# Kernel tuning notes

Measured on AMD Instinct MI355X. Metric: run time of the kernel, lower is better.

Reference implementation:

```python
import jax, jax.numpy as jnp
import numpy as np
from jax.scipy.linalg import expm

ORDER = 256
SEQ_LEN = 4096
THETA = 4096.0
MEMORY_D = 4
INPUT_SIZE = 256
HIDDEN = 512
BATCH = 8


def _lmu_AB(order):
    # Continuous-time LMU (Legendre) state-space matrices
    q = np.arange(order, dtype=np.float64)
    r = 2.0 * q + 1.0
    i, j = np.meshgrid(q, q, indexing="ij")
    A = np.where(i < j, -1.0, (-1.0) ** (i - j + 1)) * r[:, None]
    B = ((-1.0) ** q * r)[:, None]
    return A, B


def _discretize_zoh(A, B, dt=1.0):
    # ZOH via augmented matrix exponential: expm([[A,B],[0,0]]*dt)
    n = A.shape[0]
    M = np.zeros((n + 1, n + 1))
    M[:n, :n] = A * dt
    M[:n, n:] = B * dt
    Md = expm(jnp.asarray(M, dtype=jnp.float64) if jax.config.jax_enable_x64 else jnp.asarray(M, dtype=jnp.float32))
    return Md[:n, :n].astype(jnp.float32), Md[:n, n:].astype(jnp.float32)


def _impulse_H(order, seq_len, theta):
    A, B = _lmu_AB(order)
    Ad, Bd = _discretize_zoh(A / theta, B / theta, 1.0)

    def step(A_i, _):
        # H_t = A^t B ; emit A_i @ Bd then advance A_i <- Ad @ A_i
        return Ad @ A_i, (A_i @ Bd)[:, 0]

    _, Hs = jax.lax.scan(step, jnp.eye(order, dtype=jnp.float32), None, length=seq_len)
    return Hs.T  # [order, seq_len]


def setup_inputs() -> dict:
    key = jax.random.key(0)
    k1, k2, k3, k4, k5 = jax.random.split(key, 5)
    x = jax.random.normal(k1, (BATCH, SEQ_LEN, INPUT_SIZE), dtype=jnp.float32)
    Wu_w = jax.random.normal(k2, (MEMORY_D, INPUT_SIZE), dtype=jnp.float32) * (1.0 / np.sqrt(INPUT_SIZE))
    Wu_b = jax.random.normal(k3, (MEMORY_D,), dtype=jnp.float32) * 0.01
    msz = MEMORY_D * ORDER + INPUT_SIZE
    Wh_w = jax.random.normal(k4, (HIDDEN, msz), dtype=jnp.float32) * (1.0 / np.sqrt(msz))
    Wh_b = jax.random.normal(k5, (HIDDEN,), dtype=jnp.float32) * 0.01
    H = _impulse_H(ORDER, SEQ_LEN, THETA)  # exact LMU impulse response buffer
    return {"x": x, "Wu_w": Wu_w, "Wu_b": Wu_b, "Wh_w": Wh_w, "Wh_b": Wh_b, "H": H}


def reference(x, Wu_w, Wu_b, Wh_w, Wh_b, H):
    B, L, _ = x.shape
    u = jax.nn.relu(x @ Wu_w.T + Wu_b)                     # [B, L, memory_d]
    fft_u = jnp.fft.rfft(u.transpose(0, 2, 1), n=2 * L, axis=-1)   # [B, md, L+1]
    fft_H = jnp.fft.rfft(H, n=2 * L, axis=-1)              # [order, L+1]
    temp = fft_u[:, :, None, :] * fft_H[None, None, :, :]  # [B, md, order, L+1]
    m = jnp.fft.irfft(temp, n=2 * L, axis=-1)[..., :L]     # [B, md, order, L]
    m = m.reshape(B, -1, L).transpose(0, 2, 1)             # [B, L, md*order]
    input_h = jnp.concatenate([m, x], axis=-1)             # [B, L, md*order + input]
    h = jax.nn.relu(input_h @ Wh_w.T + Wh_b)               # [B, L, hidden]
    return h, h[:, -1, :]
```

## Files before the change

### kernel.cpp

```cpp
#include <hip/hip_runtime.h>

#define NB 8
#define LSEQ 4096
#define INS 256
#define MD 4
#define ORD 256
#define HID 512
#define MSZ 1280
#define FS 4128
#define NSPEC 8256
#define GMT 1056768
#define GNT 16384

#define PD(n) ((n) + ((n) >> 5))
#define LDSN 4224

typedef __attribute__((ext_vector_type(8))) short short8;
typedef __attribute__((ext_vector_type(4))) float floatx4;
typedef __attribute__((ext_vector_type(2))) float v2f;

struct ush4 { unsigned short x, y, z, w; };

__device__ v2f g_tw4096[4096];
__device__ v2f g_tw8192[4098];

__device__ __forceinline__ unsigned short f2bf(float f) {
    unsigned u = __float_as_uint(f);
    u += 0x7FFF + ((u >> 16) & 1);
    return (unsigned short)(u >> 16);
}
__device__ __forceinline__ ush4 pack4(float4 v) {
    ush4 p; p.x = f2bf(v.x); p.y = f2bf(v.y); p.z = f2bf(v.z); p.w = f2bf(v.w); return p;
}
__device__ __forceinline__ float bf2f(unsigned short s) {
    return __uint_as_float(((unsigned)s) << 16);
}

__device__ __forceinline__ v2f make2(float x, float y) { v2f r; r.x = x; r.y = y; return r; }

__device__ __forceinline__ v2f cadd(v2f a, v2f b) { return a + b; }
__device__ __forceinline__ v2f csub(v2f a, v2f b) { return a - b; }

template <int DIR>
__device__ __forceinline__ v2f jmul(v2f z) {
    const v2f s = __builtin_shufflevector(z, z, 1, 0);
    return (DIR < 0) ? s * make2(1.f, -1.f) : s * make2(-1.f, 1.f);
}

__device__ __forceinline__ v2f cmul(v2f a, v2f b) {
    const v2f byx = __builtin_shufflevector(b, b, 1, 0);
    const v2f axx = make2(a.x, a.x);
    const v2f any = make2(-a.y, a.y);
    return axx * b + any * byx;
}

template <int DIR>
__device__ __forceinline__ void bfly8(const v2f* a, v2f* b) {
    const v2f e0 = a[0] + a[4], e1 = a[0] - a[4];
    const v2f e2 = a[2] + a[6], e3 = jmul<DIR>(a[2] - a[6]);
    const v2f E0 = e0 + e2, E2 = e0 - e2;
    const v2f E1 = e1 + e3, E3 = e1 - e3;
    const v2f f0 = a[1] + a[5], f1 = a[1] - a[5];
    const v2f f2 = a[3] + a[7], f3 = jmul<DIR>(a[3] - a[7]);
    const v2f O0 = f0 + f2, O2 = f0 - f2;
    const v2f O1 = f1 + f3, O3 = f1 - f3;
    constexpr float C707 = 0.70710678118654752440f;
    const v2f W1 = make2(C707, DIR * C707);
    const v2f W3 = make2(-C707, DIR * C707);
    const v2f T1 = cmul(O1, W1);
    const v2f T2 = jmul<DIR>(O2);
    const v2f T3 = cmul(O3, W3);
    b[0] = E0 + O0; b[4] = E0 - O0;
    b[1] = E1 + T1; b[5] = E1 - T1;
    b[2] = E2 + T2; b[6] = E2 - T2;
    b[3] = E3 + T3; b[7] = E3 - T3;
}

template <int DIR, int N_, int S_>
__device__ __forceinline__ void fft_stage_ip(v2f* __restrict__ X, int tid) {
    constexpr int M_ = N_ / 8;
    constexpr int STEP = 4096 / N_;
    const int q = tid & (S_ - 1);
    const int p = tid / S_;
    const int rb = q + S_ * p;
    v2f a[8], b[8];
#pragma unroll
    for (int l = 0; l < 8; ++l) a[l] = X[PD(rb + S_ * l * M_)];

    const int pw = p * STEP;
    v2f w[7];
#pragma unroll
    for (int j = 1; j <= 7; ++j) {
        v2f t = g_tw4096[pw * j];
        if (DIR > 0) t.y = -t.y;
        w[j - 1] = t;
    }

    bfly8<DIR>(a, b);

    __syncthreads();

    const int wb = q + S_ * 8 * p;
    X[PD(wb + 0 * S_)] = b[0];
#pragma unroll
    for (int j = 1; j < 8; ++j)
        X[PD(wb + j * S_)] = cmul(b[j], w[j - 1]);
    __syncthreads();
}

extern "C" __global__ __launch_bounds__(256) void u_relu_k(
    const float* __restrict__ x, const float* __restrict__ Wuw,
    const float* __restrict__ Wub, float* __restrict__ u_t,
    unsigned short* __restrict__ x_bf,
    const float* __restrict__ Whw, unsigned short* __restrict__ Whw_bf,
    unsigned short* __restrict__ Wt) {
    const int blk = blockIdx.x;
    if (blk >= 8832) {
        if (blk < 8848) {
            const int i = (blk - 8832) * 256 + threadIdx.x;
            float sn, cs;
            sincosf(-1.53398078788564403e-3f * (float)i, &sn, &cs);
            g_tw4096[i] = make2(cs, sn);
        } else {
            const int i = (blk - 8848) * 256 + threadIdx.x;
            if (i <= 4097) {
                float sn, cs;
                sincosf(-7.66990393942820614e-4f * (float)i, &sn, &cs);
                g_tw8192[i] = make2(cs, sn);
            }
        }
        return;
    }
    if (blk >= 8704) {
        const int didx = (blk - 8704) * 1024 + threadIdx.x * 4;
        const int c = didx >> 14;
        const int r = didx & 16383;
        const int h = r >> 5, kk = r & 31;
        const float4 v = *(const float4*)(Whw + (size_t)h * MSZ + 1024 + c * 32 + kk);
        *(ush4*)(&Wt[didx]) = pack4(v);
        return;
    }
    if (blk >= 8192) {
        const int idx = (blk - 8192) * 256 + threadIdx.x;
        const int h = idx >> 8, c = idx & 255;
        const float4 v = ((const float4*)Whw)[(size_t)h * 320 + c];
        *(ush4*)(&Whw_bf[(size_t)idx * 4]) = pack4(v);
        return;
    }
    const int gid = blk * 256 + threadIdx.x;
    const int row = gid >> 6;
    const int lane = threadIdx.x & 63;
    const float4 xv = ((const float4*)x)[(size_t)row * 64 + lane];
    unsigned d0 = (unsigned)f2bf(xv.x) | ((unsigned)f2bf(xv.y) << 16);
    unsigned d1 = (unsigned)f2bf(xv.z) | ((unsigned)f2bf(xv.w) << 16);
    const unsigned e0 = (unsigned)__shfl_xor((int)d0, 1);
    const unsigned e1 = (unsigned)__shfl_xor((int)d1, 1);
    if (!(lane & 1)) {
        uint4 v; v.x = d0; v.y = d1; v.z = e0; v.w = e1;
        *(uint4*)(&x_bf[(size_t)row * 256 + lane * 4]) = v;
    }
    const float4 w0 = ((const float4*)Wuw)[0 * 64 + lane];
    const float4 w1 = ((const float4*)Wuw)[1 * 64 + lane];
    const float4 w2 = ((const float4*)Wuw)[2 * 64 + lane];
    const float4 w3 = ((const float4*)Wuw)[3 * 64 + lane];
    float a0 = xv.x * w0.x + xv.y * w0.y + xv.z * w0.z + xv.w * w0.w;
    float a1 = xv.x * w1.x + xv.y * w1.y + xv.z * w1.z + xv.w * w1.w;
    float a2 = xv.x * w2.x + xv.y * w2.y + xv.z * w2.z + xv.w * w2.w;
    float a3 = xv.x * w3.x + xv.y * w3.y + xv.z * w3.z + xv.w * w3.w;
#pragma unroll
    for (int off = 1; off < 64; off <<= 1) {
        a0 += __shfl_xor(a0, off);
        a1 += __shfl_xor(a1, off);
        a2 += __shfl_xor(a2, off);
        a3 += __shfl_xor(a3, off);
    }
    if (lane < 4) {
        float v = (lane == 0) ? a0 : (lane == 1) ? a1 : (lane == 2) ? a2 : a3;
        v = fmaxf(v + Wub[lane], 0.0f);
        const int b = row >> 12, t = row & 4095;
        u_t[((size_t)(b * 4 + lane)) * LSEQ + t] = v;
    }
}

extern "C" __global__ __launch_bounds__(512) void rfft_all_k(
    const float* __restrict__ ut, const float* __restrict__ H,
    v2f* __restrict__ fftU, unsigned short* __restrict__ fftHB) {
    __shared__ v2f A[LDSN];
    const int blk = blockIdx.x;
    const int tid = threadIdx.x;
    const bool is_u = (blk < 32);
    const float* src = is_u ? (ut + (size_t)blk * LSEQ) : (H + (size_t)(blk - 32) * LSEQ);
    const v2f* rp = (const v2f*)src;
    {
        v2f c[8], b[8];
#pragma unroll
        for (int j = 0; j < 4; ++j) c[j] = rp[tid + j * 512];
#pragma unroll
        for (int j = 4; j < 8; ++j) c[j] = make2(0.f, 0.f);
        bfly8<-1>(c, b);
        A[PD(8 * tid + 0)] = b[0];
#pragma unroll
        for (int j = 1; j < 8; ++j)
            A[PD(8 * tid + j)] = cmul(b[j], g_tw4096[tid * j]);
    }
    __syncthreads();
    fft_stage_ip<-1, 512, 8>(A, tid);
    fft_stage_ip<-1, 64, 64>(A, tid);
    fft_stage_ip<-1, 8, 512>(A, tid);
    if (is_u) {
        v2f* op = fftU + (size_t)blk * FS;
#pragma unroll
        for (int j = 0; j < 9; ++j) {
            const int k = tid + j * 512;
            if (k <= 4096) {
                const v2f Zk = A[PD(k & 4095)];
                const v2f Zm = A[PD((4096 - k) & 4095)];
                const v2f Zm2 = Zm * make2(1.f, -1.f);
                const v2f E = (Zk + Zm2) * 0.5f;
                const v2f D = (Zk - Zm2) * 0.5f;
                const v2f O = jmul<-1>(D);
                const v2f t = g_tw8192[k];
                op[k] = E + cmul(t, O);
            }
        }
    } else {
        const int o = blk - 32;
        unsigned* op = (unsigned*)(fftHB + (size_t)o * NSPEC);
#pragma unroll
        for (int j = 0; j < 9; ++j) {
            const int k = tid + j * 512;
            if (k <= 4096) {
                const v2f Zk = A[PD(k & 4095)];
                const v2f Zm = A[PD((4096 - k) & 4095)];
                const v2f Zm2 = Zm * make2(1.f, -1.f);
                const v2f E = (Zk + Zm2) * 0.5f;
                const v2f D = (Zk - Zm2) * 0.5f;
                const v2f O = jmul<-1>(D);
                const v2f t = g_tw8192[k];
                const v2f c = E + cmul(t, O);
                if (2 * k < NSPEC)
                    op[k] = (unsigned)f2bf(c.x) | ((unsigned)f2bf(c.y) << 16);
            }
        }
    }
}

extern "C" __global__ __launch_bounds__(256) void ht2_k(
    const unsigned short* __restrict__ fftHB, unsigned short* __restrict__ fftHT) {
    __shared__ unsigned short T[64 * 68];
    const int tid = threadIdx.x;
    const int s0 = blockIdx.x * 64;
    const int o0 = blockIdx.y * 64;
    const int r = tid >> 4, c4 = (tid & 15) * 4;
#pragma unroll
    for (int i = 0; i < 4; ++i) {
        const int o = r + 16 * i;
        const ush4 v = *(const ush4*)(fftHB + (size_t)(o0 + o) * NSPEC + s0 + c4);
        *(ush4*)(&T[o * 68 + c4]) = v;
    }
    __syncthreads();
#pragma unroll
    for (int i = 0; i < 4; ++i) {
        const int sl = r + 16 * i;
        const int s = s0 + sl;
        ush4 p;
        if (s < 8194) {
            p.x = T[(c4 + 0) * 68 + sl];
            p.y = T[(c4 + 1) * 68 + sl];
            p.z = T[(c4 + 2) * 68 + sl];
            p.w = T[(c4 + 3) * 68 + sl];
        } else { p.x = p.y = p.z = p.w = 0; }
        *(ush4*)(&fftHT[(size_t)s * 256 + o0 + c4]) = p;
    }
}

extern "C" __global__ __launch_bounds__(256) void g_gemm_k(
    const unsigned short* __restrict__ Whw_bf, const unsigned short* __restrict__ fftHT,
    unsigned short* __restrict__ fftG) {
    __shared__ __align__(16) char smem[36864];
    short* As = (short*)smem;
    short* Bs = (short*)(smem + 18432);
    short* Tt = (short*)smem;

    const int tid = threadIdx.x, lane = tid & 63, wave = tid >> 6;
    const int wg = blockIdx.x;
    const int loc = wg >> 3;
    const int mt = (wg & 7) * 2 + (loc & 1);
    const int nt = loc >> 1;
    const int m0 = mt * 128;
    const int n0 = nt * 128;
    floatx4 acc[2][8];
#pragma unroll
    for (int i = 0; i < 2; ++i)
#pragma unroll
        for (int j = 0; j < 8; ++j) acc[i][j] = (floatx4){0.f, 0.f, 0.f, 0.f};

    const int lr = tid >> 3;
    const int lc = (tid & 7) * 8;
    short8 ra[4], rb[4];

#define GL_A(kc, i) (*(const short8*)(Whw_bf + (size_t)((m0 + lr + 32 * (i)) >> 2) * 1024 + ((m0 + lr + 32 * (i)) & 3) * 256 + (kc) * 64 + lc))
#pragma unroll
    for (int i = 0; i < 4; ++i) {
        ra[i] = GL_A(0, i);
        const int n = n0 + lr + 32 * i;
        rb[i] = (n < NSPEC) ? *(const short8*)(fftHT + (size_t)n * 256 + lc)
                            : (short8){0, 0, 0, 0, 0, 0, 0, 0};
    }

    for (int kc = 0; kc < 4; ++kc) {
#pragma unroll
        for (int i = 0; i < 4; ++i) {
            *(short8*)(&As[(lr + 32 * i) * 72 + lc]) = ra[i];
            *(short8*)(&Bs[(lr + 32 * i) * 72 + lc]) = rb[i];
        }
        __syncthreads();
        if (kc < 3) {
#pragma unroll
            for (int i = 0; i < 4; ++i) {
                ra[i] = GL_A(kc + 1, i);
                const int n = n0 + lr + 32 * i;
                rb[i] = (n < NSPEC) ? *(const short8*)(fftHT + (size_t)n * 256 + (kc + 1) * 64 + lc)
                                    : (short8){0, 0, 0, 0, 0, 0, 0, 0};
            }
        }
        const int arow = (wave * 32 + (lane & 15)) * 72;
        const int brow = (lane & 15) * 72;
        const int kq = 8 * (lane >> 4);
#pragma unroll
        for (int kk = 0; kk < 2; ++kk) {
            const int ko = kk * 32 + kq;
            const short8 a0 = *(const short8*)(&As[arow + ko]);
            const short8 a1 = *(const short8*)(&As[arow + 16 * 72 + ko]);
#pragma unroll
            for (int nf = 0; nf < 8; ++nf) {
                const short8 bv = *(const short8*)(&Bs[brow + nf * 16 * 72 + ko]);
                acc[0][nf] = __builtin_amdgcn_mfma_f32_16x16x32_bf16(a0, bv, acc[0][nf], 0, 0, 0);
                acc[1][nf] = __builtin_amdgcn_mfma_f32_16x16x32_bf16(a1, bv, acc[1][nf], 0, 0, 0);
            }
        }
        __syncthreads();
    }
#undef GL_A
    const int wm = wave * 32;
#pragma unroll
    for (int mf = 0; mf < 2; ++mf) {
        const int row = wm + mf * 16 + 4 * (lane >> 4);
#pragma unroll
        for (int nf = 0; nf < 8; ++nf) {
            const int col = nf * 16 + (lane & 15);
#pragma unroll
            for (int r = 0; r < 4; ++r)
                Tt[(row + r) * 136 + col] = (short)f2bf(acc[mf][nf][r]);
        }
    }
    __syncthreads();
    const size_t gb = (size_t)mt * GMT + (size_t)nt * GNT;
    if (n0 < 8192) {
#pragma unroll
        for (int i = 0; i < 8; ++i) {
            const int idx = tid + i * 256;
            const int ml = idx >> 4, c8 = (idx & 15) * 8;
            const short8 v = *(const short8*)(&Tt[ml * 136 + c8]);
            *(short8*)(&fftG[gb + (size_t)idx * 8]) = v;
        }
    } else {
#pragma unroll
        for (int i = 0; i < 4; ++i) {
            const int idx = tid + i * 256;
            const int ml = idx >> 3, c8 = (idx & 7) * 8;
            const short8 v = *(const short8*)(&Tt[ml * 136 + c8]);
            *(short8*)(&fftG[gb + (size_t)idx * 8]) = v;
        }
    }
}

extern "C" __global__ __launch_bounds__(512) void conv_ifft_k(
    const v2f* __restrict__ fftU, const unsigned short* __restrict__ fftG,
    unsigned short* __restrict__ y) {
    __shared__ v2f A[LDSN];
    __shared__ v2f S4096;
    const int wg = blockIdx.x;
    const int h = ((wg & 7) << 6) + (wg >> 6);
    const int b = (wg >> 3) & 7;
    const int tid = threadIdx.x;
    const v2f* U = fftU + (size_t)b * MD * FS;
    const size_t mbase = (size_t)(h >> 5) * GMT + (size_t)((h & 31) * 4) * 128;
    const size_t tail = (size_t)(h >> 5) * GMT + (size_t)64 * GNT + (size_t)((h & 31) * 4) * 64;
#pragma unroll
    for (int j = 0; j < 9; ++j) {
        const int k = tid + j * 512;
        if (k <= 4096) {
            v2f s = make2(0.f, 0.f);
#pragma unroll
            for (int d = 0; d < MD; ++d) {
                const unsigned gv = (k < 4096)
                    ? *(const unsigned*)(fftG + mbase + (size_t)d * 128 + (size_t)(k >> 6) * GNT + (k & 63) * 2)
                    : *(const unsigned*)(fftG + tail + (size_t)d * 64);
                const v2f uu = U[d * FS + k];
                const float gx = __uint_as_float(gv << 16);
                const float gy = __uint_as_float(gv & 0xFFFF0000u);
                s.x = fmaf(uu.x, gx, fmaf(-uu.y, gy, s.x));
                s.y = fmaf(uu.x, gy, fmaf(uu.y, gx, s.y));
            }
            if (k < 4096) A[PD(k)] = s;
            else S4096 = s;
        }
    }
    __syncthreads();
    v2f c[8], bt[8];
#pragma unroll
    for (int j = 0; j < 8; ++j) {
        const int k = tid + j * 512;
        const v2f Sk = A[PD(k)];
        const v2f Sm = (k == 0) ? S4096 : A[PD(4096 - k)];
        const v2f Sm2 = Sm * make2(1.f, -1.f);
        const v2f E = (Sk + Sm2) * 0.5f;
        const v2f D = (Sk - Sm2) * 0.5f;
        const v2f t = g_tw8192[k];
        const v2f tc = t * make2(1.f, -1.f);
        const v2f O = cmul(D, tc);
        c[j] = E + jmul<1>(O);
    }
    __syncthreads();
    bfly8<1>(c, bt);
    A[PD(8 * tid + 0)] = bt[0];
#pragma unroll
    for (int j = 1; j < 8; ++j) {
        v2f t = g_tw4096[tid * j]; t.y = -t.y;
        A[PD(8 * tid + j)] = cmul(bt[j], t);
    }
    __syncthreads();
    fft_stage_ip<1, 512, 8>(A, tid);
    fft_stage_ip<1, 64, 64>(A, tid);
    {
        v2f z[8], bo[8];
#pragma unroll
        for (int k = 0; k < 8; ++k) z[k] = A[PD(tid + 512 * k)];
        bfly8<1>(z, bo);
        const float inv = 1.0f / 4096.0f;
#pragma unroll
        for (int k = 0; k < 4; ++k)
            A[PD(tid + 512 * k)] = bo[k] * inv;
    }
    __syncthreads();
    unsigned short* yp = y + (size_t)(b * HID + h) * LSEQ;
    {
        const int q = tid;
        unsigned dw[4];
#pragma unroll
        for (int jj = 0; jj < 4; ++jj) {
            const v2f z = A[PD(4 * q + jj)];
            dw[jj] = (unsigned)f2bf(z.x) | ((unsigned)f2bf(z.y) << 16);
        }
        uint4 v; v.x = dw[0]; v.y = dw[1]; v.z = dw[2]; v.w = dw[3];
        *(uint4*)(yp + 8 * q) = v;
    }
}

extern "C" __global__ __launch_bounds__(256) void out_gemm_k(
    const unsigned short* __restrict__ x_bf, const unsigned short* __restrict__ Wt,
    const float* __restrict__ Whb, const unsigned short* __restrict__ y,
    float* __restrict__ out) {
    __shared__ __align__(16) char smem[66560];
    short* As = (short*)smem;
    short* Bs = (short*)(smem + 2560);
    float* Whbs = (float*)smem;
    short* Ys = (short*)(smem + 2560);
    float* Ct = (float*)smem;

    const int tid = threadIdx.x, lane = tid & 63, wave = tid >> 6;
    const int wg = blockIdx.x;
    const int s = ((wg & 7) << 7) + (wg >> 3);
    const int m0 = s * 32;
    const int b = m0 >> 12;
    const int t0 = m0 & 4095;
    const int hq = wave * 128;

    floatx4 acc[2][8];
#pragma unroll
    for (int i = 0; i < 2; ++i)
#pragma unroll
        for (int j = 0; j < 8; ++j) acc[i][j] = (floatx4){0.f, 0.f, 0.f, 0.f};

    short8 ra, rb[8];
    const int arow = tid >> 2, acb = (tid & 3) * 8;
    if (tid < 128) ra = *(const short8*)(x_bf + (size_t)(m0 + arow) * INS + acb);
#pragma unroll
    for (int j = 0; j < 8; ++j)
        rb[j] = *(const short8*)(Wt + (size_t)tid * 64 + j * 8);

    for (int c = 0; c < 8; ++c) {
        if (tid < 128) *(short8*)(&As[arow * 40 + acb]) = ra;
#pragma unroll
        for (int j = 0; j < 8; ++j)
            *(short8*)(&Bs[(2 * tid + (j >> 2)) * 40 + (j & 3) * 8]) = rb[j];
        __syncthreads();
        if (c < 7) {
            if (tid < 128) ra = *(const short8*)(x_bf + (size_t)(m0 + arow) * INS + (c + 1) * 32 + acb);
#pragma unroll
            for (int j = 0; j < 8; ++j)
                rb[j] = *(const short8*)(Wt + (size_t)(c + 1) * 16384 + (size_t)tid * 64 + j * 8);
        }
        const int kq = 8 * (lane >> 4);
        const short8 a0 = *(const short8*)(&As[(lane & 15) * 40 + kq]);
        const short8 a1 = *(const short8*)(&As[((lane & 15) + 16) * 40 + kq]);
#pragma unroll
        for (int nf = 0; nf < 8; ++nf) {
            const short8 bv = *(const short8*)(&Bs[(hq + nf * 16 + (lane & 15)) * 40 + kq]);
            acc[0][nf] = __builtin_amdgcn_mfma_f32_16x16x32_bf16(a0, bv, acc[0][nf], 0, 0, 0);
            acc[1][nf] = __builtin_amdgcn_mfma_f32_16x16x32_bf16(a1, bv, acc[1][nf], 0, 0, 0);
        }
        __syncthreads();
    }

    Whbs[tid] = Whb[tid];
    Whbs[tid + 256] = Whb[tid + 256];
#pragma unroll
    for (int i = 0; i < 16; ++i) {
        const int idx = tid + i * 256;
        const int hh = idx >> 3, tq = (idx & 7) * 4;
        const ush4 v = *(const ush4*)(y + (size_t)(b * HID + hh) * LSEQ + t0 + tq);
        *(ush4*)(&Ys[hh * 36 + tq]) = v;
    }
    __syncthreads();
#pragma unroll
    for (int nf = 0; nf < 8; ++nf) {
        const int hh = hq + nf * 16 + (lane & 15);
        const float bias = Whbs[hh];
#pragma unroll
        for (int mf = 0; mf < 2; ++mf)
#pragma unroll
            for (int r = 0; r < 4; ++r) {
                const int row = mf * 16 + 4 * (lane >> 4) + r;
                acc[mf][nf][r] = fmaxf(acc[mf][nf][r] + bf2f(Ys[hh * 36 + row]) + bias, 0.f);
            }
    }
    __syncthreads();
#pragma unroll
    for (int nf = 0; nf < 8; ++nf) {
        const int col = hq + nf * 16 + (lane & 15);
#pragma unroll
        for (int mf = 0; mf < 2; ++mf)
#pragma unroll
            for (int r = 0; r < 4; ++r) {
                const int row = mf * 16 + 4 * (lane >> 4) + r;
                Ct[row * 520 + col] = acc[mf][nf][r];
            }
    }
    __syncthreads();
#pragma unroll
    for (int i = 0; i < 16; ++i) {
        const int idx = tid + i * 256;
        const int row = idx >> 7, c4 = (idx & 127) * 4;
        const floatx4 t = *(const floatx4*)&Ct[row * 520 + c4];
        *(floatx4*)(out + (size_t)(m0 + row) * HID + c4) = t;
        if (((m0 + row) & 4095) == 4095)
            *(floatx4*)(out + (size_t)NB * LSEQ * HID + (size_t)b * HID + c4) = t;
    }
}

extern "C" void kernel_launch(void* const* d_in, const int* in_sizes, int n_in,
                              void* d_out, int out_size, void* d_ws, size_t ws_size,
                              hipStream_t stream) {
    const float* x   = (const float*)d_in[0];
    const float* Wuw = (const float*)d_in[1];
    const float* Wub = (const float*)d_in[2];
    const float* Whw = (const float*)d_in[3];
    const float* Whb = (const float*)d_in[4];
    const float* H   = (const float*)d_in[5];
    char* wsb = (char*)d_ws;
    unsigned short* fftG   = (unsigned short*)(wsb);
    unsigned short* yb     = (unsigned short*)(wsb + 33816576);
    v2f*            fftU   = (v2f*)(wsb + 67371008);
    unsigned short* fftHT  = (unsigned short*)(wsb + 68427776);
    float*          ut     = (float*)(wsb + 72654848);
    unsigned short* x_bf   = (unsigned short*)(wsb + 73179136);
    unsigned short* Whw_bf = (unsigned short*)(wsb + 89956352);
    unsigned short* Wt     = (unsigned short*)(wsb + 91004928);
    unsigned short* fftHB  = (unsigned short*)(wsb + 91267072);
    float* out = (float*)d_out;

    hipLaunchKernelGGL(u_relu_k, dim3(8865), dim3(256), 0, stream, x, Wuw, Wub, ut, x_bf, Whw, Whw_bf, Wt);
    hipLaunchKernelGGL(rfft_all_k, dim3(288), dim3(512), 0, stream, ut, H, fftU, fftHB);
    hipLaunchKernelGGL(ht2_k, dim3(129, 4), dim3(256), 0, stream, fftHB, fftHT);
    hipLaunchKernelGGL(g_gemm_k, dim3(1040), dim3(256), 0, stream, Whw_bf, fftHT, fftG);
    hipLaunchKernelGGL(conv_ifft_k, dim3(4096), dim3(512), 0, stream, fftU, fftG, yb);
    hipLaunchKernelGGL(out_gemm_k, dim3(1024), dim3(256), 0, stream, x_bf, Wt, Whb, yb, out);
}
```

Baseline: 246.7 us.

## Regroup prep kernels into stages and use packed f32/bf16 conversion instructions

Regroups the front-end launches. A small prep kernel converts the weights and builds the twiddle tables. The H rfft now runs in the same launch as the x projection and bf16 conversion, and the u rfft runs with the H spectrum transpose. This overlaps independent work, keeps the launch count the same, and drops one dependency barrier between launches. It also swaps manual bf16 rounding for v_cvt_pk_bf16_f32 and uses inline-asm packed add/fma in the butterflies, which may limit compiler scheduling.

```diff
diff --git a/kernel.cpp b/kernel.cpp
--- a/kernel.cpp
+++ b/kernel.cpp
@@ -35,18 +35,27 @@
 __device__ __forceinline__ float bf2f(unsigned short s) {
     return __uint_as_float(((unsigned)s) << 16);
 }
+__device__ __forceinline__ unsigned cvt_pk_bf16(float lo, float hi) {
+    unsigned r;
+    asm("v_cvt_pk_bf16_f32 %0, %1, %2" : "=v"(r) : "v"(lo), "v"(hi));
+    return r;
+}
 
 __device__ __forceinline__ v2f make2(float x, float y) { v2f r; r.x = x; r.y = y; return r; }
 
-__device__ __forceinline__ v2f cadd(v2f a, v2f b) { return a + b; }
-__device__ __forceinline__ v2f csub(v2f a, v2f b) { return a - b; }
+__device__ __forceinline__ v2f padd(v2f a, v2f b) {
+    v2f r; asm("v_pk_add_f32 %0, %1, %2" : "=v"(r) : "v"(a), "v"(b)); return r;
+}
+__device__ __forceinline__ v2f psub(v2f a, v2f b) {
+    const v2f m1 = make2(-1.f, -1.f);
+    v2f r; asm("v_pk_fma_f32 %0, %1, %2, %3" : "=v"(r) : "v"(b), "v"(m1), "v"(a)); return r;
+}
 
 template <int DIR>
 __device__ __forceinline__ v2f jmul(v2f z) {
     const v2f s = __builtin_shufflevector(z, z, 1, 0);
     return (DIR < 0) ? s * make2(1.f, -1.f) : s * make2(-1.f, 1.f);
 }
-
 __device__ __forceinline__ v2f cmul(v2f a, v2f b) {
     const v2f byx = __builtin_shufflevector(b, b, 1, 0);
     const v2f axx = make2(a.x, a.x);
@@ -56,24 +65,24 @@
 
 template <int DIR>
 __device__ __forceinline__ void bfly8(const v2f* a, v2f* b) {
-    const v2f e0 = a[0] + a[4], e1 = a[0] - a[4];
-    const v2f e2 = a[2] + a[6], e3 = jmul<DIR>(a[2] - a[6]);
-    const v2f E0 = e0 + e2, E2 = e0 - e2;
-    const v2f E1 = e1 + e3, E3 = e1 - e3;
-    const v2f f0 = a[1] + a[5], f1 = a[1] - a[5];
-    const v2f f2 = a[3] + a[7], f3 = jmul<DIR>(a[3] - a[7]);
-    const v2f O0 = f0 + f2, O2 = f0 - f2;
-    const v2f O1 = f1 + f3, O3 = f1 - f3;
+    const v2f e0 = padd(a[0], a[4]), e1 = psub(a[0], a[4]);
+    const v2f e2 = padd(a[2], a[6]), e3 = jmul<DIR>(psub(a[2], a[6]));
+    const v2f E0 = padd(e0, e2), E2 = psub(e0, e2);
+    const v2f E1 = padd(e1, e3), E3 = psub(e1, e3);
+    const v2f f0 = padd(a[1], a[5]), f1 = psub(a[1], a[5]);
+    const v2f f2 = padd(a[3], a[7]), f3 = jmul<DIR>(psub(a[3], a[7]));
+    const v2f O0 = padd(f0, f2), O2 = psub(f0, f2);
+    const v2f O1 = padd(f1, f3), O3 = psub(f1, f3);
     constexpr float C707 = 0.70710678118654752440f;
     const v2f W1 = make2(C707, DIR * C707);
     const v2f W3 = make2(-C707, DIR * C707);
     const v2f T1 = cmul(O1, W1);
     const v2f T2 = jmul<DIR>(O2);
     const v2f T3 = cmul(O3, W3);
-    b[0] = E0 + O0; b[4] = E0 - O0;
-    b[1] = E1 + T1; b[5] = E1 - T1;
-    b[2] = E2 + T2; b[6] = E2 - T2;
-    b[3] = E3 + T3; b[7] = E3 - T3;
+    b[0] = padd(E0, O0); b[4] = psub(E0, O0);
+    b[1] = padd(E1, T1); b[5] = psub(E1, T1);
+    b[2] = padd(E2, T2); b[6] = psub(E2, T2);
+    b[3] = padd(E3, T3); b[7] = psub(E3, T3);
 }
 
 template <int DIR, int N_, int S_>
@@ -108,51 +117,88 @@
     __syncthreads();
 }
 
-extern "C" __global__ __launch_bounds__(256) void u_relu_k(
-    const float* __restrict__ x, const float* __restrict__ Wuw,
-    const float* __restrict__ Wub, float* __restrict__ u_t,
-    unsigned short* __restrict__ x_bf,
+extern "C" __global__ __launch_bounds__(256) void prep_k(
     const float* __restrict__ Whw, unsigned short* __restrict__ Whw_bf,
     unsigned short* __restrict__ Wt) {
     const int blk = blockIdx.x;
-    if (blk >= 8832) {
-        if (blk < 8848) {
-            const int i = (blk - 8832) * 256 + threadIdx.x;
-            float sn, cs;
-            sincosf(-1.53398078788564403e-3f * (float)i, &sn, &cs);
-            g_tw4096[i] = make2(cs, sn);
-        } else {
-            const int i = (blk - 8848) * 256 + threadIdx.x;
-            if (i <= 4097) {
-                float sn, cs;
-                sincosf(-7.66990393942820614e-4f * (float)i, &sn, &cs);
-                g_tw8192[i] = make2(cs, sn);
-            }
-        }
-        return;
-    }
-    if (blk >= 8704) {
-        const int didx = (blk - 8704) * 1024 + threadIdx.x * 4;
+    if (blk < 512) {
+        const int idx = blk * 256 + threadIdx.x;
+        const int h = idx >> 8, c = idx & 255;
+        const float4 v = ((const float4*)Whw)[(size_t)h * 320 + c];
+        *(ush4*)(&Whw_bf[(size_t)idx * 4]) = pack4(v);
+    } else if (blk < 640) {
+        const int didx = (blk - 512) * 1024 + threadIdx.x * 4;
         const int c = didx >> 14;
         const int r = didx & 16383;
         const int h = r >> 5, kk = r & 31;
         const float4 v = *(const float4*)(Whw + (size_t)h * MSZ + 1024 + c * 32 + kk);
         *(ush4*)(&Wt[didx]) = pack4(v);
+    } else if (blk < 656) {
+        const int i = (blk - 640) * 256 + threadIdx.x;
+        float sn, cs;
+        sincosf(-1.53398078788564403e-3f * (float)i, &sn, &cs);
+        g_tw4096[i] = make2(cs, sn);
+    } else {
+        const int i = (blk - 656) * 256 + threadIdx.x;
+        if (i <= 4097) {
+            float sn, cs;
+            sincosf(-7.66990393942820614e-4f * (float)i, &sn, &cs);
+            g_tw8192[i] = make2(cs, sn);
+        }
+    }
+}
+
+extern "C" __global__ __launch_bounds__(512) void stage1_k(
+    const float* __restrict__ x, const float* __restrict__ Wuw,
+    const float* __restrict__ Wub, float* __restrict__ u_t,
+    unsigned short* __restrict__ x_bf,
+    const float* __restrict__ H, unsigned short* __restrict__ fftHB) {
+    const int blk = blockIdx.x;
+    const int tid = threadIdx.x;
+    if (blk < 256) {
+        __shared__ v2f A[LDSN];
+        const int o = blk;
+        const v2f* rp = (const v2f*)(H + (size_t)o * LSEQ);
+        {
+            v2f c[8], b[8];
+#pragma unroll
+            for (int j = 0; j < 4; ++j) c[j] = rp[tid + j * 512];
+#pragma unroll
+            for (int j = 4; j < 8; ++j) c[j] = make2(0.f, 0.f);
+            bfly8<-1>(c, b);
+            A[PD(8 * tid + 0)] = b[0];
+#pragma unroll
+            for (int j = 1; j < 8; ++j)
+                A[PD(8 * tid + j)] = cmul(b[j], g_tw4096[tid * j]);
+        }
+        __syncthreads();
+        fft_stage_ip<-1, 512, 8>(A, tid);
+        fft_stage_ip<-1, 64, 64>(A, tid);
+        fft_stage_ip<-1, 8, 512>(A, tid);
+        unsigned* op = (unsigned*)(fftHB + (size_t)o * NSPEC);
+#pragma unroll
+        for (int j = 0; j < 9; ++j) {
+            const int k = tid + j * 512;
+            if (k <= 4096) {
+                const v2f Zk = A[PD(k & 4095)];
+                const v2f Zm = A[PD((4096 - k) & 4095)];
+                const v2f Zm2 = Zm * make2(1.f, -1.f);
+                const v2f E = padd(Zk, Zm2) * 0.5f;
+                const v2f D = psub(Zk, Zm2) * 0.5f;
+                const v2f O = jmul<-1>(D);
+                const v2f t = g_tw8192[k];
+                const v2f c = padd(E, cmul(t, O));
+                if (2 * k < NSPEC)
+                    op[k] = cvt_pk_bf16(c.x, c.y);
+            }
+        }
         return;
     }
-    if (blk >= 8192) {
-        const int idx = (blk - 8192) * 256 + threadIdx.x;
-        const int h = idx >> 8, c = idx & 255;
-        const float4 v = ((const float4*)Whw)[(size_t)h * 320 + c];
-        *(ush4*)(&Whw_bf[(size_t)idx * 4]) = pack4(v);
-        return;
-    }
-    const int gid = blk * 256 + threadIdx.x;
-    const int row = gid >> 6;
-    const int lane = threadIdx.x & 63;
+    const int row = (blk - 256) * 8 + (tid >> 6);
+    const int lane = tid & 63;
     const float4 xv = ((const float4*)x)[(size_t)row * 64 + lane];
-    unsigned d0 = (unsigned)f2bf(xv.x) | ((unsigned)f2bf(xv.y) << 16);
-    unsigned d1 = (unsigned)f2bf(xv.z) | ((unsigned)f2bf(xv.w) << 16);
+    unsigned d0 = cvt_pk_bf16(xv.x, xv.y);
+    unsigned d1 = cvt_pk_bf16(xv.z, xv.w);
     const unsigned e0 = (unsigned)__shfl_xor((int)d0, 1);
     const unsigned e1 = (unsigned)__shfl_xor((int)d1, 1);
     if (!(lane & 1)) {
@@ -182,32 +228,30 @@
     }
 }
 
-extern "C" __global__ __launch_bounds__(512) void rfft_all_k(
-    const float* __restrict__ ut, const float* __restrict__ H,
-    v2f* __restrict__ fftU, unsigned short* __restrict__ fftHB) {
-    __shared__ v2f A[LDSN];
+extern "C" __global__ __launch_bounds__(512) void stage2_k(
+    const float* __restrict__ ut, v2f* __restrict__ fftU,
+    const unsigned short* __restrict__ fftHB, unsigned short* __restrict__ fftHT) {
     const int blk = blockIdx.x;
     const int tid = threadIdx.x;
-    const bool is_u = (blk < 32);
-    const float* src = is_u ? (ut + (size_t)blk * LSEQ) : (H + (size_t)(blk - 32) * LSEQ);
-    const v2f* rp = (const v2f*)src;
-    {
-        v2f c[8], b[8];
-#pragma unroll
-        for (int j = 0; j < 4; ++j) c[j] = rp[tid + j * 512];
-#pragma unroll
-        for (int j = 4; j < 8; ++j) c[j] = make2(0.f, 0.f);
-        bfly8<-1>(c, b);
-        A[PD(8 * tid + 0)] = b[0];
-#pragma unroll
-        for (int j = 1; j < 8; ++j)
-            A[PD(8 * tid + j)] = cmul(b[j], g_tw4096[tid * j]);
-    }
-    __syncthreads();
-    fft_stage_ip<-1, 512, 8>(A, tid);
-    fft_stage_ip<-1, 64, 64>(A, tid);
-    fft_stage_ip<-1, 8, 512>(A, tid);
-    if (is_u) {
+    if (blk < 32) {
+        __shared__ v2f A[LDSN];
+        const v2f* rp = (const v2f*)(ut + (size_t)blk * LSEQ);
+        {
+            v2f c[8], b[8];
+#pragma unroll
+            for (int j = 0; j < 4; ++j) c[j] = rp[tid + j * 512];
+#pragma unroll
+            for (int j = 4; j < 8; ++j) c[j] = make2(0.f, 0.f);
+            bfly8<-1>(c, b);
+            A[PD(8 * tid + 0)] = b[0];
+#pragma unroll
+            for (int j = 1; j < 8; ++j)
+                A[PD(8 * tid + j)] = cmul(b[j], g_tw4096[tid * j]);
+        }
+        __syncthreads();
+        fft_stage_ip<-1, 512, 8>(A, tid);
+        fft_stage_ip<-1, 64, 64>(A, tid);
+        fft_stage_ip<-1, 8, 512>(A, tid);
         v2f* op = fftU + (size_t)blk * FS;
 #pragma unroll
         for (int j = 0; j < 9; ++j) {
@@ -216,47 +260,27 @@
                 const v2f Zk = A[PD(k & 4095)];
                 const v2f Zm = A[PD((4096 - k) & 4095)];
                 const v2f Zm2 = Zm * make2(1.f, -1.f);
-                const v2f E = (Zk + Zm2) * 0.5f;
-                const v2f D = (Zk - Zm2) * 0.5f;
+                const v2f E = padd(Zk, Zm2) * 0.5f;
+                const v2f D = psub(Zk, Zm2) * 0.5f;
                 const v2f O = jmul<-1>(D);
                 const v2f t = g_tw8192[k];
-                op[k] = E + cmul(t, O);
+                op[k] = padd(E, cmul(t, O));
             }
         }
-    } else {
-        const int o = blk - 32;
-        unsigned* op = (unsigned*)(fftHB + (size_t)o * NSPEC);
-#pragma unroll
-        for (int j = 0; j < 9; ++j) {
-            const int k = tid + j * 512;
-            if (k <= 4096) {
-                const v2f Zk = A[PD(k & 4095)];
-                const v2f Zm = A[PD((4096 - k) & 4095)];
-                const v2f Zm2 = Zm * make2(1.f, -1.f);
-                const v2f E = (Zk + Zm2) * 0.5f;
-                const v2f D = (Zk - Zm2) * 0.5f;
-                const v2f O = jmul<-1>(D);
-                const v2f t = g_tw8192[k];
-                const v2f c = E + cmul(t, O);
-                if (2 * k < NSPEC)
-                    op[k] = (unsigned)f2bf(c.x) | ((unsigned)f2bf(c.y) << 16);
-            }
-        }
-    }
-}
-
-extern "C" __global__ __launch_bounds__(256) void ht2_k(
-    const unsigned short* __restrict__ fftHB, unsigned short* __restrict__ fftHT) {
-    __shared__ unsigned short T[64 * 68];
-    const int tid = threadIdx.x;
-    const int s0 = blockIdx.x * 64;
-    const int o0 = blockIdx.y * 64;
-    const int r = tid >> 4, c4 = (tid & 15) * 4;
+        return;
+    }
+    __shared__ unsigned short T[2][64 * 68];
+    const int sub = tid >> 8;
+    const int tt = tid & 255;
+    const int t = (blk - 32) * 2 + sub;
+    const int s0 = (t % 129) * 64;
+    const int o0 = (t / 129) * 64;
+    const int r = tt >> 4, c4 = (tt & 15) * 4;
 #pragma unroll
     for (int i = 0; i < 4; ++i) {
         const int o = r + 16 * i;
         const ush4 v = *(const ush4*)(fftHB + (size_t)(o0 + o) * NSPEC + s0 + c4);
-        *(ush4*)(&T[o * 68 + c4]) = v;
+        *(ush4*)(&T[sub][o * 68 + c4]) = v;
     }
     __syncthreads();
 #pragma unroll
@@ -265,10 +289,10 @@
         const int s = s0 + sl;
         ush4 p;
         if (s < 8194) {
-            p.x = T[(c4 + 0) * 68 + sl];
-            p.y = T[(c4 + 1) * 68 + sl];
-            p.z = T[(c4 + 2) * 68 + sl];
-            p.w = T[(c4 + 3) * 68 + sl];
+            p.x = T[sub][(c4 + 0) * 68 + sl];
+            p.y = T[sub][(c4 + 1) * 68 + sl];
+            p.z = T[sub][(c4 + 2) * 68 + sl];
+            p.w = T[sub][(c4 + 3) * 68 + sl];
         } else { p.x = p.y = p.z = p.w = 0; }
         *(ush4*)(&fftHT[(size_t)s * 256 + o0 + c4]) = p;
     }
@@ -415,12 +439,12 @@
         const v2f Sk = A[PD(k)];
         const v2f Sm = (k == 0) ? S4096 : A[PD(4096 - k)];
         const v2f Sm2 = Sm * make2(1.f, -1.f);
-        const v2f E = (Sk + Sm2) * 0.5f;
-        const v2f D = (Sk - Sm2) * 0.5f;
+        const v2f E = padd(Sk, Sm2) * 0.5f;
+        const v2f D = psub(Sk, Sm2) * 0.5f;
         const v2f t = g_tw8192[k];
         const v2f tc = t * make2(1.f, -1.f);
         const v2f O = cmul(D, tc);
-        c[j] = E + jmul<1>(O);
+        c[j] = padd(E, jmul<1>(O));
     }
     __syncthreads();
     bfly8<1>(c, bt);
@@ -451,7 +475,7 @@
 #pragma unroll
         for (int jj = 0; jj < 4; ++jj) {
             const v2f z = A[PD(4 * q + jj)];
-            dw[jj] = (unsigned)f2bf(z.x) | ((unsigned)f2bf(z.y) << 16);
+            dw[jj] = cvt_pk_bf16(z.x, z.y);
         }
         uint4 v; v.x = dw[0]; v.y = dw[1]; v.z = dw[2]; v.w = dw[3];
         *(uint4*)(yp + 8 * q) = v;
@@ -581,9 +605,9 @@
     unsigned short* fftHB  = (unsigned short*)(wsb + 91267072);
     float* out = (float*)d_out;
 
-    hipLaunchKernelGGL(u_relu_k, dim3(8865), dim3(256), 0, stream, x, Wuw, Wub, ut, x_bf, Whw, Whw_bf, Wt);
-    hipLaunchKernelGGL(rfft_all_k, dim3(288), dim3(512), 0, stream, ut, H, fftU, fftHB);
-    hipLaunchKernelGGL(ht2_k, dim3(129, 4), dim3(256), 0, stream, fftHB, fftHT);
+    hipLaunchKernelGGL(prep_k, dim3(673), dim3(256), 0, stream, Whw, Whw_bf, Wt);
+    hipLaunchKernelGGL(stage1_k, dim3(4352), dim3(512), 0, stream, x, Wuw, Wub, ut, x_bf, H, fftHB);
+    hipLaunchKernelGGL(stage2_k, dim3(290), dim3(512), 0, stream, ut, fftU, fftHB, fftHT);
     hipLaunchKernelGGL(g_gemm_k, dim3(1040), dim3(256), 0, stream, Whw_bf, fftHT, fftG);
     hipLaunchKernelGGL(conv_ifft_k, dim3(4096), dim3(512), 0, stream, fftU, fftG, yb);
     hipLaunchKernelGGL(out_gemm_k, dim3(1024), dim3(256), 0, stream, x_bf, Wt, Whb, yb, out);
```

Measured after the change: 249.0 us. Within noise of the previous version (+0.9%).
